# Kernel optimization log

Hardware: AMD Instinct MI355X
Metric: run time of the kernel (lower is better)

The kernel has to match this reference:

```python
import jax, jax.numpy as jnp
import numpy as np

N_HEADS = 16
HIDDEN = 1024
HEAD_SIZE = HIDDEN // N_HEADS  # 64
BATCH = 2
SEQ_LEN = 2048


def setup_inputs() -> dict:
    key = jax.random.key(0)
    k1, k2, k3 = jax.random.split(key, 3)
    x = jax.random.normal(k1, (BATCH, SEQ_LEN, HIDDEN), dtype=jnp.float32)
    # nn.Linear(hidden, 3*hidden): store weight as [in, out] for x @ W
    W_qkv = jax.random.normal(k2, (HIDDEN, 3 * HIDDEN), dtype=jnp.float32) * (HIDDEN ** -0.5)
    b_qkv = jax.random.normal(k3, (3 * HIDDEN,), dtype=jnp.float32) * 0.02
    return {"x": x, "W_qkv": W_qkv, "b_qkv": b_qkv}


def reference(x, W_qkv, b_qkv):
    B, T, D = x.shape
    nh, hs = N_HEADS, HEAD_SIZE
    scale = hs ** -0.5

    # qkv projection, then the module's exact (unusual) reshape:
    # [B,T,3D] viewed as [3,B,T,hs,nh], permuted to [3,B,nh,T,hs]
    y = x @ W_qkv + b_qkv                      # [B, T, 3D]
    qkv = y.reshape(3, B, T, hs, nh).transpose(0, 1, 4, 2, 3)  # [3,B,nh,T,hs]
    q, k, v = qkv[0], qkv[1], qkv[2]

    # KV-cache scatter with arange index over the full seq is an identity write;
    # cache.transpose(1,2) returns k, v unchanged.

    scores = jnp.einsum('bhtd,bhsd->bhts', q, k) * scale       # [B,nh,T,T]
    causal = jnp.tril(jnp.ones((T, T), dtype=bool))
    scores = jnp.where(causal[None, None], scores, -jnp.inf)
    attn = jax.nn.softmax(scores, axis=-1)
    ctx = jnp.einsum('bhts,bhsd->bhtd', attn, v)               # [B,nh,T,hs]
    # rearrange 'b h t d -> b t (h d)'; note self.o is NOT applied in forward
    return ctx.transpose(0, 2, 1, 3).reshape(B, T, nh * hs)
```

## Files before the change

### kernel.cpp

```cpp
#include <hip/hip_runtime.h>
#include <hip/hip_bf16.h>

typedef __attribute__((ext_vector_type(8))) short s8v;
typedef __attribute__((ext_vector_type(4))) short s4v;
typedef __attribute__((ext_vector_type(4))) float f4v;

__device__ __forceinline__ void g2lds16(const void* g, void* l) {
  __builtin_amdgcn_global_load_lds(
      (__attribute__((address_space(1))) void*)(g),
      (__attribute__((address_space(3))) void*)(l), 16, 0, 0);
}

__device__ __forceinline__ short f2bf(float f) {
  __hip_bfloat16 h = __float2bfloat16(f);
  return *reinterpret_cast<short*>(&h);
}

__global__ void k_prep(const float* __restrict__ x, const float* __restrict__ W,
                       __hip_bfloat16* __restrict__ xb, __hip_bfloat16* __restrict__ Wt) {
  int bx = blockIdx.x;
  if (bx < 4096) {
    int i = (bx * 256 + threadIdx.x) * 4;
    float4 v = *(const float4*)(x + i);
    __hip_bfloat16 o[4] = {__float2bfloat16(v.x), __float2bfloat16(v.y),
                           __float2bfloat16(v.z), __float2bfloat16(v.w)};
    *(uint2*)(xb + i) = *(const uint2*)(o);
  } else {
    __shared__ float tile[32][33];
    int r = bx - 4096;
    int rt = r / 96;
    int ct = r - rt * 96;
    int c0 = ct * 32, r0 = rt * 32;
    int tr = threadIdx.x >> 5, tc = threadIdx.x & 31;
#pragma unroll
    for (int i = 0; i < 32; i += 8)
      tile[tr + i][tc] = W[(size_t)(r0 + tr + i) * 3072 + c0 + tc];
    __syncthreads();
#pragma unroll
    for (int i = 0; i < 32; i += 8)
      Wt[(size_t)(c0 + tr + i) * 1024 + r0 + tc] = __float2bfloat16(tile[tc][tr + i]);
  }
}

__global__ __launch_bounds__(256) void k_gemm(const __hip_bfloat16* __restrict__ A,
                                              const __hip_bfloat16* __restrict__ Bt,
                                              const float* __restrict__ bias,
                                              __hip_bfloat16* __restrict__ Q,
                                              __hip_bfloat16* __restrict__ K,
                                              __hip_bfloat16* __restrict__ Vt) {
  __shared__ __align__(16) __hip_bfloat16 As[2][128 * 32];
  __shared__ __align__(16) __hip_bfloat16 Bs[2][128 * 32];
  const int tid = threadIdx.x;
  const int lane = tid & 63, wave = tid >> 6;
  const int m0 = blockIdx.y * 128, n0 = blockIdx.x * 128;
  const int wm = (wave & 1) * 64, wn = (wave >> 1) * 64;
  const int lrow = lane & 15;
  const int quad = lane >> 4;

  f4v acc[4][4] = {};

  auto stage = [&](int k0, int kb) {
#pragma unroll
    for (int c = 0; c < 2; ++c) {
      int e = c * 2048 + tid * 8;
      int row = e >> 5;
      int slot = (e & 31) >> 3;
      int src = k0 + ((slot ^ ((row >> 1) & 3)) << 3);
      g2lds16(A + (size_t)(m0 + row) * 1024 + src, &As[kb][e]);
      g2lds16(Bt + (size_t)(n0 + row) * 1024 + src, &Bs[kb][e]);
    }
  };

  const int swz = (quad ^ ((lrow >> 1) & 3)) * 8;

  stage(0, 0);
  for (int it = 0; it < 32; ++it) {
    __syncthreads();
    if (it < 31) stage((it + 1) * 32, (it + 1) & 1);
    const __hip_bfloat16* Ab = As[it & 1];
    const __hip_bfloat16* Bb = Bs[it & 1];
    s8v af[4], bfr[4];
#pragma unroll
    for (int mi = 0; mi < 4; ++mi) af[mi] = *(const s8v*)(Ab + (wm + mi * 16 + lrow) * 32 + swz);
#pragma unroll
    for (int ni = 0; ni < 4; ++ni) bfr[ni] = *(const s8v*)(Bb + (wn + ni * 16 + lrow) * 32 + swz);
#pragma unroll
    for (int mi = 0; mi < 4; ++mi)
#pragma unroll
      for (int ni = 0; ni < 4; ++ni)
        acc[mi][ni] = __builtin_amdgcn_mfma_f32_16x16x32_bf16(af[mi], bfr[ni], acc[mi][ni], 0, 0, 0);
  }

  const int cw = n0 + wn;
  const int c10 = cw >> 10;
  const int d0 = (cw & 1023) >> 4;
  const int h = lrow;
  float bv[4];
#pragma unroll
  for (int ni = 0; ni < 4; ++ni) bv[ni] = bias[cw + ni * 16 + lrow];

#pragma unroll
  for (int mi = 0; mi < 4; ++mi) {
    int rbase = m0 + wm + mi * 16 + quad * 4;
#pragma unroll
    for (int reg = 0; reg < 4; ++reg) {
      int rr = rbase + reg;
      int u = 3 * rr + c10;
      int s = u >> 12;
      int b = (u >> 11) & 1;
      int t = u & 2047;
      if (s < 2) {
        __hip_bfloat16* dst = (s == 0) ? Q : K;
        const float qs = (s == 0) ? 0.18033688011112042f : 1.0f;
        s4v pk;
#pragma unroll
        for (int ni = 0; ni < 4; ++ni) pk[ni] = f2bf((acc[mi][ni][reg] + bv[ni]) * qs);
        *(s4v*)(dst + ((size_t)(b * 16 + h) * 2048 + t) * 64 + d0) = pk;
      } else {
#pragma unroll
        for (int ni = 0; ni < 4; ++ni)
          Vt[((size_t)(b * 16 + h) * 64 + d0 + ni) * 2048 + t] =
              __float2bfloat16(acc[mi][ni][reg] + bv[ni]);
      }
    }
  }
}

__global__ __launch_bounds__(256, 3) void k_attn(const __hip_bfloat16* __restrict__ Q,
                                                 const __hip_bfloat16* __restrict__ K,
                                                 const __hip_bfloat16* __restrict__ Vt,
                                                 float* __restrict__ out) {
  __shared__ __align__(16) char lds[2][16384];

  const int tid = threadIdx.x;
  const int lane = tid & 63, w = tid >> 6;
  const int l = lane & 15, q = lane >> 4, lx = l & 7;

  const int bid = blockIdx.x;
  const int xcd = bid & 7;
  const int idx = bid >> 3;
  const int bh = xcd + 8 * (idx & 3);
  const int qb = 31 - (idx >> 2);

  const char* Kb = (const char*)(K + (size_t)bh * 131072);
  const char* Vb = (const char*)(Vt + (size_t)bh * 131072);
  const __hip_bfloat16* Qp = Q + (size_t)bh * 131072 + (size_t)qb * 4096;

  s8v Qf[2];
#pragma unroll
  for (int kh = 0; kh < 2; ++kh)
    Qf[kh] = *(const s8v*)(Qp + (size_t)(w * 16 + l) * 64 + kh * 32 + q * 8);

  f4v O[4] = {};
  float m = -INFINITY, lsum = 0.f;
  const int tg = qb * 64 + w * 16 + l;

  auto stage = [&](int j, char* buf) {
#pragma unroll
    for (int c = 0; c < 4; ++c) {
      int chunk = w * 4 + c;
      int ls = chunk * 64 + lane;
      if (chunk < 8) {
        int row = ls >> 3, kb = ls & 7;
        g2lds16(Kb + (size_t)j * 8192 + row * 128 + ((kb ^ (row & 7)) << 4),
                buf + ls * 16);
      } else {
        int ls2 = ls - 512;
        int d = ls2 >> 3, kb = ls2 & 7;
        g2lds16(Vb + (size_t)d * 4096 + (size_t)j * 128 + ((kb ^ (d & 7)) << 4),
                buf + 8192 + ls2 * 16);
      }
    }
  };

  stage(0, lds[0]);
  __syncthreads();

  for (int j = 0; j <= qb; ++j) {
    const char* Kl = lds[j & 1];
    const char* Vl = Kl + 8192;
    if (j < qb) stage(j + 1, lds[(j + 1) & 1]);

    f4v S[4];
#pragma unroll
    for (int nt = 0; nt < 4; ++nt) {
      const char* rowp = Kl + (nt * 16 + l) * 128;
      s8v k0 = *(const s8v*)(rowp + ((q ^ lx) << 4));
      s8v k1 = *(const s8v*)(rowp + (((4 + q) ^ lx) << 4));
      f4v z = {0.f, 0.f, 0.f, 0.f};
      z = __builtin_amdgcn_mfma_f32_16x16x32_bf16(k0, Qf[0], z, 0, 0, 0);
      z = __builtin_amdgcn_mfma_f32_16x16x32_bf16(k1, Qf[1], z, 0, 0, 0);
      S[nt] = z;
    }

    if (j == qb) {
#pragma unroll
      for (int nt = 0; nt < 4; ++nt)
#pragma unroll
        for (int r = 0; r < 4; ++r)
          if (j * 64 + nt * 16 + q * 4 + r > tg) S[nt][r] = -1e30f;
    }

    float mx = S[0][0];
#pragma unroll
    for (int nt = 0; nt < 4; ++nt)
#pragma unroll
      for (int r = 0; r < 4; ++r) mx = fmaxf(mx, S[nt][r]);
    mx = fmaxf(mx, __shfl_xor(mx, 16));
    mx = fmaxf(mx, __shfl_xor(mx, 32));

    if (!__all(mx - m <= 8.f)) {
      float mn = fmaxf(m, mx);
      float alpha = exp2f(m - mn);
      m = mn;
      lsum *= alpha;
#pragma unroll
      for (int dt = 0; dt < 4; ++dt) O[dt] *= alpha;
    }

    float rs = 0.f;
    s4v Pf[4];
#pragma unroll
    for (int nt = 0; nt < 4; ++nt)
#pragma unroll
      for (int r = 0; r < 4; ++r) {
        float e = exp2f(S[nt][r] - m);
        rs += e;
        Pf[nt][r] = f2bf(e);
      }
    rs += __shfl_xor(rs, 16);
    rs += __shfl_xor(rs, 32);
    lsum += rs;

#pragma unroll
    for (int sc = 0; sc < 4; ++sc) {
      int so = ((sc * 2 + (q >> 1)) ^ lx) * 16 + (q & 1) * 8;
#pragma unroll
      for (int dt = 0; dt < 4; ++dt) {
        s4v vv = *(const s4v*)(Vl + (dt * 16 + l) * 128 + so);
        O[dt] = __builtin_amdgcn_mfma_f32_16x16x16bf16_1k(vv, Pf[sc], O[dt], 0, 0, 0);
      }
    }
    __syncthreads();
  }

  float inv = 1.f / lsum;
  int b = bh >> 4, h = bh & 15;
  float* ob = out + ((size_t)b * 2048 + tg) * 1024 + h * 64;
#pragma unroll
  for (int dt = 0; dt < 4; ++dt) {
    f4v val = O[dt] * inv;
    *(f4v*)(ob + dt * 16 + q * 4) = val;
  }
}

extern "C" void kernel_launch(void* const* d_in, const int* in_sizes, int n_in,
                              void* d_out, int out_size, void* d_ws, size_t ws_size,
                              hipStream_t stream) {
  const float* x = (const float*)d_in[0];
  const float* W = (const float*)d_in[1];
  const float* bias = (const float*)d_in[2];
  float* out = (float*)d_out;

  char* ws = (char*)d_ws;
  __hip_bfloat16* xb = (__hip_bfloat16*)ws;
  __hip_bfloat16* Wt = (__hip_bfloat16*)(ws + 8388608);
  __hip_bfloat16* Qg = (__hip_bfloat16*)(ws + 14680064);
  __hip_bfloat16* Kg = (__hip_bfloat16*)(ws + 23068672);
  __hip_bfloat16* Vt = (__hip_bfloat16*)(ws + 31457280);

  k_prep<<<7168, 256, 0, stream>>>(x, W, xb, Wt);
  k_gemm<<<dim3(24, 32), 256, 0, stream>>>(xb, Wt, bias, Qg, Kg, Vt);
  k_attn<<<1024, 256, 0, stream>>>(Qg, Kg, Vt, out);
}
```

Measured before the change: 175.0 us.

## Fuse prep, GEMM and attention into one cooperative persistent kernel with grid syncs

Merges the three kernels into one cooperative launch of 768 blocks that run the prep, GEMM and attention phases in turn, separated by grid-wide barriers, so two kernel launch gaps go away. The attention work is redistributed: blocks 512 and up each take a second unit. The original three-kernel path is kept as a fallback if the cooperative launch fails. Risks include grid.sync cost, lost occupancy from the combined kernel's register and LDS footprint, and a worse attention load balance, since one block handles two causal units while every block must be co-resident.

```diff
diff --git a/kernel.cpp b/kernel.cpp
--- a/kernel.cpp
+++ b/kernel.cpp
@@ -1,5 +1,8 @@
 #include <hip/hip_runtime.h>
 #include <hip/hip_bf16.h>
+#include <hip/hip_cooperative_groups.h>
+
+namespace cg = cooperative_groups;
 
 typedef __attribute__((ext_vector_type(8))) short s8v;
 typedef __attribute__((ext_vector_type(4))) short s4v;
@@ -16,43 +19,42 @@
   return *reinterpret_cast<short*>(&h);
 }
 
-__global__ void k_prep(const float* __restrict__ x, const float* __restrict__ W,
-                       __hip_bfloat16* __restrict__ xb, __hip_bfloat16* __restrict__ Wt) {
-  int bx = blockIdx.x;
-  if (bx < 4096) {
-    int i = (bx * 256 + threadIdx.x) * 4;
+
+__device__ __forceinline__ void prep_unit(int u, int tid, char* smem,
+    const float* __restrict__ x, const float* __restrict__ W,
+    __hip_bfloat16* __restrict__ xb, __hip_bfloat16* __restrict__ Wt) {
+  if (u < 4096) {
+    int i = (u * 256 + tid) * 4;
     float4 v = *(const float4*)(x + i);
     __hip_bfloat16 o[4] = {__float2bfloat16(v.x), __float2bfloat16(v.y),
                            __float2bfloat16(v.z), __float2bfloat16(v.w)};
     *(uint2*)(xb + i) = *(const uint2*)(o);
   } else {
-    __shared__ float tile[32][33];
-    int r = bx - 4096;
+    float (*tile)[33] = (float(*)[33])smem;
+    int r = u - 4096;
     int rt = r / 96;
     int ct = r - rt * 96;
     int c0 = ct * 32, r0 = rt * 32;
-    int tr = threadIdx.x >> 5, tc = threadIdx.x & 31;
-#pragma unroll
-    for (int i = 0; i < 32; i += 8)
-      tile[tr + i][tc] = W[(size_t)(r0 + tr + i) * 3072 + c0 + tc];
+    int tr = tid >> 5, tc = tid & 31;
     __syncthreads();
 #pragma unroll
-    for (int i = 0; i < 32; i += 8)
-      Wt[(size_t)(c0 + tr + i) * 1024 + r0 + tc] = __float2bfloat16(tile[tc][tr + i]);
-  }
-}
-
-__global__ __launch_bounds__(256) void k_gemm(const __hip_bfloat16* __restrict__ A,
-                                              const __hip_bfloat16* __restrict__ Bt,
-                                              const float* __restrict__ bias,
-                                              __hip_bfloat16* __restrict__ Q,
-                                              __hip_bfloat16* __restrict__ K,
-                                              __hip_bfloat16* __restrict__ Vt) {
-  __shared__ __align__(16) __hip_bfloat16 As[2][128 * 32];
-  __shared__ __align__(16) __hip_bfloat16 Bs[2][128 * 32];
-  const int tid = threadIdx.x;
+    for (int ii = 0; ii < 32; ii += 8)
+      tile[tr + ii][tc] = W[(size_t)(r0 + tr + ii) * 3072 + c0 + tc];
+    __syncthreads();
+#pragma unroll
+    for (int ii = 0; ii < 32; ii += 8)
+      Wt[(size_t)(c0 + tr + ii) * 1024 + r0 + tc] = __float2bfloat16(tile[tc][tr + ii]);
+  }
+}
+
+__device__ __forceinline__ void gemm_body(int bid, int tid, char* smem,
+    const __hip_bfloat16* __restrict__ A, const __hip_bfloat16* __restrict__ Bt,
+    const float* __restrict__ bias, __hip_bfloat16* __restrict__ Q,
+    __hip_bfloat16* __restrict__ K, __hip_bfloat16* __restrict__ Vt) {
+  __hip_bfloat16* As = (__hip_bfloat16*)smem;
+  __hip_bfloat16* Bs = (__hip_bfloat16*)(smem + 16384);
   const int lane = tid & 63, wave = tid >> 6;
-  const int m0 = blockIdx.y * 128, n0 = blockIdx.x * 128;
+  const int m0 = (bid / 24) * 128, n0 = (bid % 24) * 128;
   const int wm = (wave & 1) * 64, wn = (wave >> 1) * 64;
   const int lrow = lane & 15;
   const int quad = lane >> 4;
@@ -66,8 +68,8 @@
       int row = e >> 5;
       int slot = (e & 31) >> 3;
       int src = k0 + ((slot ^ ((row >> 1) & 3)) << 3);
-      g2lds16(A + (size_t)(m0 + row) * 1024 + src, &As[kb][e]);
-      g2lds16(Bt + (size_t)(n0 + row) * 1024 + src, &Bs[kb][e]);
+      g2lds16(A + (size_t)(m0 + row) * 1024 + src, As + kb * 4096 + e);
+      g2lds16(Bt + (size_t)(n0 + row) * 1024 + src, Bs + kb * 4096 + e);
     }
   };
 
@@ -77,8 +79,8 @@
   for (int it = 0; it < 32; ++it) {
     __syncthreads();
     if (it < 31) stage((it + 1) * 32, (it + 1) & 1);
-    const __hip_bfloat16* Ab = As[it & 1];
-    const __hip_bfloat16* Bb = Bs[it & 1];
+    const __hip_bfloat16* Ab = As + (it & 1) * 4096;
+    const __hip_bfloat16* Bb = Bs + (it & 1) * 4096;
     s8v af[4], bfr[4];
 #pragma unroll
     for (int mi = 0; mi < 4; ++mi) af[mi] = *(const s8v*)(Ab + (wm + mi * 16 + lrow) * 32 + swz);
@@ -126,19 +128,17 @@
   }
 }
 
-__global__ __launch_bounds__(256, 3) void k_attn(const __hip_bfloat16* __restrict__ Q,
-                                                 const __hip_bfloat16* __restrict__ K,
-                                                 const __hip_bfloat16* __restrict__ Vt,
-                                                 float* __restrict__ out) {
-  __shared__ __align__(16) char lds[2][16384];
-
-  const int tid = threadIdx.x;
+__device__ __forceinline__ void attn_unit(int unit, int tid, char* smem,
+    const __hip_bfloat16* __restrict__ Q, const __hip_bfloat16* __restrict__ K,
+    const __hip_bfloat16* __restrict__ Vt, float* __restrict__ out) {
+  char* l0 = smem;
+  char* l1 = smem + 16384;
+
   const int lane = tid & 63, w = tid >> 6;
   const int l = lane & 15, q = lane >> 4, lx = l & 7;
 
-  const int bid = blockIdx.x;
-  const int xcd = bid & 7;
-  const int idx = bid >> 3;
+  const int xcd = unit & 7;
+  const int idx = unit >> 3;
   const int bh = xcd + 8 * (idx & 3);
   const int qb = 31 - (idx >> 2);
 
@@ -173,13 +173,13 @@
     }
   };
 
-  stage(0, lds[0]);
+  stage(0, l0);
   __syncthreads();
 
   for (int j = 0; j <= qb; ++j) {
-    const char* Kl = lds[j & 1];
+    const char* Kl = (j & 1) ? l1 : l0;
     const char* Vl = Kl + 8192;
-    if (j < qb) stage(j + 1, lds[(j + 1) & 1]);
+    if (j < qb) stage(j + 1, ((j + 1) & 1) ? l1 : l0);
 
     f4v S[4];
 #pragma unroll
@@ -245,13 +245,62 @@
   }
 
   float inv = 1.f / lsum;
-  int b = bh >> 4, h = bh & 15;
-  float* ob = out + ((size_t)b * 2048 + tg) * 1024 + h * 64;
+  int b = bh >> 4, hh = bh & 15;
+  float* ob = out + ((size_t)b * 2048 + tg) * 1024 + hh * 64;
 #pragma unroll
   for (int dt = 0; dt < 4; ++dt) {
     f4v val = O[dt] * inv;
     *(f4v*)(ob + dt * 16 + q * 4) = val;
   }
+}
+
+__global__ __launch_bounds__(256, 4) void k_fused(
+    const float* __restrict__ x, const float* __restrict__ W,
+    const float* __restrict__ bias, float* __restrict__ out,
+    __hip_bfloat16* __restrict__ xb, __hip_bfloat16* __restrict__ Wt,
+    __hip_bfloat16* __restrict__ Q, __hip_bfloat16* __restrict__ K,
+    __hip_bfloat16* __restrict__ Vt) {
+  __shared__ __align__(16) char smem[32768];
+  const int tid = threadIdx.x;
+  const int bid = blockIdx.x;
+  cg::grid_group grid = cg::this_grid();
+
+  for (int u = bid; u < 7168; u += 768) prep_unit(u, tid, smem, x, W, xb, Wt);
+
+  __threadfence();
+  grid.sync();
+
+  gemm_body(bid, tid, smem, xb, Wt, bias, Q, K, Vt);
+
+  __threadfence();
+  grid.sync();
+
+  attn_unit(bid, tid, smem, Q, K, Vt, out);
+  if (bid >= 512) attn_unit(bid + 256, tid, smem, Q, K, Vt, out);
+}
+
+__global__ void k_prep(const float* __restrict__ x, const float* __restrict__ W,
+                       __hip_bfloat16* __restrict__ xb, __hip_bfloat16* __restrict__ Wt) {
+  __shared__ __align__(16) char smem[4224];
+  prep_unit(blockIdx.x, threadIdx.x, smem, x, W, xb, Wt);
+}
+
+__global__ __launch_bounds__(256) void k_gemm(const __hip_bfloat16* __restrict__ A,
+                                              const __hip_bfloat16* __restrict__ Bt,
+                                              const float* __restrict__ bias,
+                                              __hip_bfloat16* __restrict__ Q,
+                                              __hip_bfloat16* __restrict__ K,
+                                              __hip_bfloat16* __restrict__ Vt) {
+  __shared__ __align__(16) char smem[32768];
+  gemm_body(blockIdx.x, threadIdx.x, smem, A, Bt, bias, Q, K, Vt);
+}
+
+__global__ __launch_bounds__(256, 3) void k_attn(const __hip_bfloat16* __restrict__ Q,
+                                                 const __hip_bfloat16* __restrict__ K,
+                                                 const __hip_bfloat16* __restrict__ Vt,
+                                                 float* __restrict__ out) {
+  __shared__ __align__(16) char smem[32768];
+  attn_unit(blockIdx.x, threadIdx.x, smem, Q, K, Vt, out);
 }
 
 extern "C" void kernel_launch(void* const* d_in, const int* in_sizes, int n_in,
@@ -267,9 +316,15 @@
   __hip_bfloat16* Wt = (__hip_bfloat16*)(ws + 8388608);
   __hip_bfloat16* Qg = (__hip_bfloat16*)(ws + 14680064);
   __hip_bfloat16* Kg = (__hip_bfloat16*)(ws + 23068672);
-  __hip_bfloat16* Vt = (__hip_bfloat16*)(ws + 31457280);
-
-  k_prep<<<7168, 256, 0, stream>>>(x, W, xb, Wt);
-  k_gemm<<<dim3(24, 32), 256, 0, stream>>>(xb, Wt, bias, Qg, Kg, Vt);
-  k_attn<<<1024, 256, 0, stream>>>(Qg, Kg, Vt, out);
-}
+  __hip_bfloat16* Vtp = (__hip_bfloat16*)(ws + 31457280);
+
+  void* args[9] = {(void*)&x, (void*)&W, (void*)&bias, (void*)&out,
+                   (void*)&xb, (void*)&Wt, (void*)&Qg, (void*)&Kg, (void*)&Vtp};
+  hipError_t err = hipLaunchCooperativeKernel(k_fused, dim3(768), dim3(256),
+                                              args, 0u, stream);
+  if (err != hipSuccess) {
+    k_prep<<<7168, 256, 0, stream>>>(x, W, xb, Wt);
+    k_gemm<<<768, 256, 0, stream>>>(xb, Wt, bias, Qg, Kg, Vtp);
+    k_attn<<<1024, 256, 0, stream>>>(Qg, Kg, Vtp, out);
+  }
+}
```

After: 534.4 us. 205% more time.
